# Kernel optimization log

Measured on AMD Instinct MI355X. Metric: run time of the kernel, lower is better.

Reference implementation:

```python
import jax, jax.numpy as jnp
import numpy as np

B, K, D, NH = 4096, 32, 1024, 16
HD = D // NH
LN_EPS = 1e-5
RMS_EPS = 1e-6


def layernorm(x, g, b):
    mu = jnp.mean(x, axis=-1, keepdims=True)
    var = jnp.mean((x - mu) ** 2, axis=-1, keepdims=True)
    return (x - mu) * jax.lax.rsqrt(var + LN_EPS) * g + b


def rmsnorm(x, g):
    ms = jnp.mean(x ** 2, axis=-1, keepdims=True)
    return x * jax.lax.rsqrt(ms + RMS_EPS) * g


def setup_inputs() -> dict:
    key = jax.random.key(0)
    ks = jax.random.split(key, 12)
    s = 0.02
    inp = {
        "query": jax.random.normal(ks[0], (B, D), jnp.float32),
        "point_features": jax.random.normal(ks[1], (B, K, D), jnp.float32),
        "lnq_g": jnp.ones((D,), jnp.float32),
        "lnq_b": jnp.zeros((D,), jnp.float32),
        "lnkv_g": jnp.ones((D,), jnp.float32),
        "lnkv_b": jnp.zeros((D,), jnp.float32),
        "Wq": jax.random.normal(ks[2], (D, D), jnp.float32) * s,
        "bq": jnp.zeros((D,), jnp.float32),
        "Wk": jax.random.normal(ks[3], (D, D), jnp.float32) * s,
        "bk": jnp.zeros((D,), jnp.float32),
        "Wv": jax.random.normal(ks[4], (D, D), jnp.float32) * s,
        "bv": jnp.zeros((D,), jnp.float32),
        "rmsq_g": jnp.ones((D,), jnp.float32),
        "rmsk_g": jnp.ones((D,), jnp.float32),
        "Wo": jax.random.normal(ks[5], (D, D), jnp.float32) * s,
        "bo": jnp.zeros((D,), jnp.float32),
        "mlpn_g": jnp.ones((D,), jnp.float32),
        "mlpn_b": jnp.zeros((D,), jnp.float32),
        "W1": jax.random.normal(ks[6], (D, 4 * D), jnp.float32) * s,
        "b1": jnp.zeros((4 * D,), jnp.float32),
        "W2": jax.random.normal(ks[7], (4 * D, D), jnp.float32) * s,
        "b2": jnp.zeros((D,), jnp.float32),
    }
    return inp


def reference(query, point_features, lnq_g, lnq_b, lnkv_g, lnkv_b,
              Wq, bq, Wk, bk, Wv, bv, rmsq_g, rmsk_g, Wo, bo,
              mlpn_g, mlpn_b, W1, b1, W2, b2):
    q_in = layernorm(query, lnq_g, lnq_b)            # [B, D]
    kv_in = layernorm(point_features, lnkv_g, lnkv_b)  # [B, K, D]

    q = rmsnorm(q_in @ Wq + bq, rmsq_g)              # [B, D]
    k = rmsnorm(kv_in @ Wk + bk, rmsk_g)             # [B, K, D]
    v = kv_in @ Wv + bv                               # [B, K, D]

    # Faithful to original: raw row-major reshape [B,K,D] -> [B,NH,K,HD]
    qh = q.reshape(B, NH, HD)                         # [B, NH, HD] (q_len = 1)
    kh = k.reshape(B, NH, K, HD)
    vh = v.reshape(B, NH, K, HD)

    scores = jnp.einsum('bhd,bhkd->bhk', qh, kh) / np.sqrt(HD).astype(np.float32)
    attn = jax.nn.softmax(scores, axis=-1)            # [B, NH, K]
    out = jnp.einsum('bhk,bhkd->bhd', attn, vh)       # [B, NH, HD]

    # Faithful: transpose(1,2) then reshape -> [B, HD, NH] -> [B, D]
    out = jnp.transpose(out, (0, 2, 1)).reshape(B, D)
    out = (out @ Wo + bo) + query                     # residual

    h = layernorm(out, mlpn_g, mlpn_b)
    mlp_out = (jax.nn.gelu(h @ W1 + b1, approximate=False) @ W2) + b2
    return out + mlp_out
```

## Files before the change

### kernel.cpp

```cpp
#include <hip/hip_runtime.h>
#include <stdint.h>

#define DEVI __device__ __forceinline__

typedef unsigned short u16;
typedef short s8v __attribute__((ext_vector_type(8)));
typedef float f4v __attribute__((ext_vector_type(4)));
typedef u16 u16x4 __attribute__((ext_vector_type(4)));

DEVI u16 f2bf(float f) {
  unsigned u = __float_as_uint(f);
  u += 0x7fffu + ((u >> 16) & 1u);
  return (u16)(u >> 16);
}
DEVI float bf2f(u16 h) { return __uint_as_float(((unsigned)h) << 16); }

DEVI void gload16(const void* g, void* l) {
  __builtin_amdgcn_global_load_lds(
      (const __attribute__((address_space(1))) void*)(uintptr_t)g,
      (__attribute__((address_space(3))) void*)(uintptr_t)l, 16, 0, 0);
}

__global__ __launch_bounds__(256) void transpose_w(const float* __restrict__ W,
                                                   u16* __restrict__ Wt, int R, int C) {
  __shared__ float tile[32][33];
  const int tx = threadIdx.x & 31, ty = threadIdx.x >> 5;
  const int r0 = blockIdx.y * 32, c0 = blockIdx.x * 32;
#pragma unroll
  for (int i = 0; i < 4; ++i)
    tile[ty + 8 * i][tx] = W[(size_t)(r0 + ty + 8 * i) * C + c0 + tx];
  __syncthreads();
#pragma unroll
  for (int i = 0; i < 4; ++i)
    Wt[(size_t)(c0 + ty + 8 * i) * R + r0 + tx] = f2bf(tile[tx][ty + 8 * i]);
}

__global__ __launch_bounds__(256) void ln_rows(const float* __restrict__ x,
                                               const float* __restrict__ g,
                                               const float* __restrict__ bsh,
                                               u16* __restrict__ y) {
  const size_t row = blockIdx.x;
  const int t = threadIdx.x;
  float4 v = ((const float4*)(x + row * 1024))[t];
  float s = v.x + v.y + v.z + v.w;
  float q = v.x * v.x + v.y * v.y + v.z * v.z + v.w * v.w;
#pragma unroll
  for (int m = 1; m < 64; m <<= 1) { s += __shfl_xor(s, m); q += __shfl_xor(q, m); }
  __shared__ float sh[8];
  if ((t & 63) == 0) { sh[t >> 6] = s; sh[4 + (t >> 6)] = q; }
  __syncthreads();
  s = sh[0] + sh[1] + sh[2] + sh[3];
  q = sh[4] + sh[5] + sh[6] + sh[7];
  const float mu = s * (1.f / 1024.f);
  const float var = q * (1.f / 1024.f) - mu * mu;
  const float rs = rsqrtf(var + 1e-5f);
  const int c = t * 4;
  const float in[4] = {v.x, v.y, v.z, v.w};
  u16x4 o;
#pragma unroll
  for (int i = 0; i < 4; ++i) o[i] = f2bf((in[i] - mu) * rs * g[c + i] + bsh[c + i]);
  *(u16x4*)(y + row * 1024 + c) = o;
}

__global__ __launch_bounds__(256) void qrms_k(const float* __restrict__ x,
                                              const float* __restrict__ gq,
                                              u16* __restrict__ y) {
  const size_t row = blockIdx.x;
  const int t = threadIdx.x;
  float4 v = ((const float4*)(x + row * 1024))[t];
  float q = v.x * v.x + v.y * v.y + v.z * v.z + v.w * v.w;
#pragma unroll
  for (int m = 1; m < 64; m <<= 1) q += __shfl_xor(q, m);
  __shared__ float sh[4];
  if ((t & 63) == 0) sh[t >> 6] = q;
  __syncthreads();
  q = sh[0] + sh[1] + sh[2] + sh[3];
  const float rs = rsqrtf(q * (1.f / 1024.f) + 1e-6f) * 0.125f;
  const int c = t * 4;
  const float in[4] = {v.x, v.y, v.z, v.w};
  u16x4 o;
#pragma unroll
  for (int i = 0; i < 4; ++i) o[i] = f2bf(in[i] * rs * gq[c + i]);
  *(u16x4*)(y + row * 1024 + c) = o;
}

template <int EPI>
__global__ __launch_bounds__(512, 2) void gemm256(
    const u16* __restrict__ A, const u16* __restrict__ Bt,
    const float* __restrict__ biasK, const float* __restrict__ biasV,
    const float* __restrict__ gcol, u16* __restrict__ CK, u16* __restrict__ CV,
    float* __restrict__ rowssq, int M, int N, int K, int RB) {
  __shared__ u16 lds[4][16384];
  const int t = threadIdx.x;
  const int lane = t & 63;
  const int wave = t >> 6;
  const int wm = wave >> 2, wn = wave & 3;
  const int fr = lane & 15, kq = lane >> 4;

  const int bid = blockIdx.x;
  const int cpx = gridDim.x >> 3;
  const int swz = (bid & 7) * cpx + (bid >> 3);
  const int rb = swz % RB, cb = swz / RB;
  const size_t row0 = (size_t)rb * 256, col0 = (size_t)cb * 256;

  f4v acc[8][4];
#pragma unroll
  for (int i = 0; i < 8; ++i)
#pragma unroll
    for (int n = 0; n < 4; ++n) acc[i][n] = (f4v){0.f, 0.f, 0.f, 0.f};

  const u16* Ag0 = A + (row0 + (t >> 2)) * (size_t)K + (t & 3) * 8;
  const u16* Ag1 = Ag0 + (size_t)128 * K;
  const u16* Bg0 = Bt + (col0 + (t >> 2)) * (size_t)K + (t & 3) * 8;
  const u16* Bg1 = Bg0 + (size_t)128 * K;

  const int NT = K >> 5;

#pragma unroll
  for (int tt = 0; tt < 3; ++tt) {
    u16* sA = &lds[tt][0];
    u16* sB = &lds[tt][8192];
    gload16(Ag0 + tt * 32, sA + t * 8);
    gload16(Ag1 + tt * 32, sA + 4096 + t * 8);
    gload16(Bg0 + tt * 32, sB + t * 8);
    gload16(Bg1 + tt * 32, sB + 4096 + t * 8);
  }

#pragma unroll 4
  for (int T = 0; T < NT; ++T) {
    asm volatile("s_waitcnt vmcnt(8)" ::: "memory");
    __builtin_amdgcn_s_barrier();
    __builtin_amdgcn_sched_barrier(0);
    const u16* sA = &lds[T & 3][0];
    const u16* sB = &lds[T & 3][8192];
    s8v a[4], b[4];
#pragma unroll
    for (int m = 0; m < 4; ++m)
      a[m] = *(const s8v*)&sA[(wm * 128 + m * 16 + fr) * 32 + kq * 8];
#pragma unroll
    for (int n = 0; n < 4; ++n)
      b[n] = *(const s8v*)&sB[(wn * 64 + n * 16 + fr) * 32 + kq * 8];
    if (T + 3 < NT) {
      u16* dA = &lds[(T + 3) & 3][0];
      gload16(Ag0 + (T + 3) * 32, dA + t * 8);
      gload16(Ag1 + (T + 3) * 32, dA + 4096 + t * 8);
    }
    __builtin_amdgcn_s_setprio(1);
#pragma unroll
    for (int m = 0; m < 4; ++m)
#pragma unroll
      for (int n = 0; n < 4; ++n)
        acc[m][n] = __builtin_amdgcn_mfma_f32_16x16x32_bf16(a[m], b[n], acc[m][n], 0, 0, 0);
    __builtin_amdgcn_s_setprio(0);
    __builtin_amdgcn_s_barrier();
#pragma unroll
    for (int m = 0; m < 4; ++m)
      a[m] = *(const s8v*)&sA[(wm * 128 + 64 + m * 16 + fr) * 32 + kq * 8];
    if (T + 3 < NT) {
      u16* dB = &lds[(T + 3) & 3][8192];
      gload16(Bg0 + (T + 3) * 32, dB + t * 8);
      gload16(Bg1 + (T + 3) * 32, dB + 4096 + t * 8);
    }
    __builtin_amdgcn_s_setprio(1);
#pragma unroll
    for (int m = 0; m < 4; ++m)
#pragma unroll
      for (int n = 0; n < 4; ++n)
        acc[4 + m][n] = __builtin_amdgcn_mfma_f32_16x16x32_bf16(a[m], b[n], acc[4 + m][n], 0, 0, 0);
    __builtin_amdgcn_s_setprio(0);
  }

  const int kq4 = kq * 4;
  if (EPI == 0) {
    const bool isK = (col0 < 1024);
    if (isK) {
#pragma unroll
      for (int ai = 0; ai < 8; ++ai) {
        int cols[4];
        float bb[4], gg[4];
#pragma unroll
        for (int n = 0; n < 4; ++n) {
          cols[n] = (int)col0 + wn * 64 + n * 16 + fr;
          bb[n] = biasK[cols[n]];
          gg[n] = gcol[cols[n]];
        }
#pragma unroll
        for (int r = 0; r < 4; ++r) {
          const size_t grow = row0 + wm * 128 + ai * 16 + kq4 + r;
          float v[4];
#pragma unroll
          for (int n = 0; n < 4; ++n) v[n] = acc[ai][n][r] + bb[n];
          float s = v[0] * v[0] + v[1] * v[1] + v[2] * v[2] + v[3] * v[3];
          s += __shfl_xor(s, 1);
          s += __shfl_xor(s, 2);
          s += __shfl_xor(s, 4);
          s += __shfl_xor(s, 8);
          if (fr == 0) atomicAdd(&rowssq[grow], s);
#pragma unroll
          for (int n = 0; n < 4; ++n)
            CK[grow * 1024 + cols[n]] = f2bf(v[n] * gg[n]);
        }
      }
    } else {
#pragma unroll
      for (int ai = 0; ai < 8; ++ai) {
        int cols[4];
        float bb[4];
#pragma unroll
        for (int n = 0; n < 4; ++n) {
          cols[n] = (int)col0 - 1024 + wn * 64 + n * 16 + fr;
          bb[n] = biasV[cols[n]];
        }
#pragma unroll
        for (int r = 0; r < 4; ++r) {
          const size_t grow = row0 + wm * 128 + ai * 16 + kq4 + r;
#pragma unroll
          for (int n = 0; n < 4; ++n)
            CV[grow * 1024 + cols[n]] = f2bf(acc[ai][n][r] + bb[n]);
        }
      }
    }
  } else {
#pragma unroll
    for (int ai = 0; ai < 8; ++ai) {
      int cols[4];
      float bb[4];
#pragma unroll
      for (int n = 0; n < 4; ++n) {
        cols[n] = (int)col0 + wn * 64 + n * 16 + fr;
        bb[n] = biasK[cols[n]];
      }
#pragma unroll
      for (int r = 0; r < 4; ++r) {
        const size_t grow = row0 + wm * 128 + ai * 16 + kq4 + r;
#pragma unroll
        for (int n = 0; n < 4; ++n) {
          const float x = acc[ai][n][r] + bb[n];
          CK[grow * (size_t)N + cols[n]] = f2bf(0.5f * x * (1.f + erff(x * 0.70710678118654752f)));
        }
      }
    }
  }
}

template <int EPI>
__global__ __launch_bounds__(256) void gemm_bt(
    const u16* __restrict__ A, const u16* __restrict__ Bt,
    const float* __restrict__ bias, const float* __restrict__ gcol,
    void* __restrict__ Cv, const float* __restrict__ extra,
    float* __restrict__ rowssq, int M, int N, int K) {
  __shared__ u16 As[128 * 32];
  __shared__ u16 Bs[128 * 32];
  const int t = threadIdx.x;
  const int lane = t & 63;
  const int wave = t >> 6;
  const int wr = wave >> 1, wc = wave & 1;
  const size_t row0 = (size_t)blockIdx.y * 128;
  const size_t col0 = (size_t)blockIdx.x * 128;

  f4v acc[4][4];
#pragma unroll
  for (int m = 0; m < 4; ++m)
#pragma unroll
    for (int n = 0; n < 4; ++n) acc[m][n] = (f4v){0.f, 0.f, 0.f, 0.f};

  const int sr = t >> 2;
  const int sc = (t & 3) * 8;
  const u16* Ag = A + (row0 + sr) * (size_t)K + sc;
  const u16* Bg = Bt + (col0 + sr) * (size_t)K + sc;
  u16* Al = &As[sr * 32 + sc];
  u16* Bl = &Bs[sr * 32 + sc];
  const int fr = lane & 15;
  const int kg = (lane >> 4) * 8;

  for (int k0 = 0; k0 < K; k0 += 32) {
    gload16(Ag + k0, Al);
    gload16(Ag + k0 + (size_t)64 * K, Al + 64 * 32);
    gload16(Bg + k0, Bl);
    gload16(Bg + k0 + (size_t)64 * K, Bl + 64 * 32);
    __syncthreads();
    s8v a[4], b[4];
#pragma unroll
    for (int m = 0; m < 4; ++m)
      a[m] = *(const s8v*)&As[(wr * 64 + m * 16 + fr) * 32 + kg];
#pragma unroll
    for (int n = 0; n < 4; ++n)
      b[n] = *(const s8v*)&Bs[(wc * 64 + n * 16 + fr) * 32 + kg];
#pragma unroll
    for (int m = 0; m < 4; ++m)
#pragma unroll
      for (int n = 0; n < 4; ++n)
        acc[m][n] = __builtin_amdgcn_mfma_f32_16x16x32_bf16(a[m], b[n], acc[m][n], 0, 0, 0);
    __syncthreads();
  }

  const int rg = (lane >> 4) * 4;
#pragma unroll
  for (int m = 0; m < 4; ++m) {
    int cols[4];
    float bvals[4];
#pragma unroll
    for (int n = 0; n < 4; ++n) {
      cols[n] = (int)col0 + wc * 64 + n * 16 + fr;
      bvals[n] = bias[cols[n]];
    }
#pragma unroll
    for (int r = 0; r < 4; ++r) {
      const size_t grow = row0 + wr * 64 + m * 16 + rg + r;
      float v[4];
#pragma unroll
      for (int n = 0; n < 4; ++n) v[n] = acc[m][n][r] + bvals[n];
#pragma unroll
      for (int n = 0; n < 4; ++n) {
        const size_t idx = grow * (size_t)N + cols[n];
        if (EPI == 0) {
          ((float*)Cv)[idx] = v[n];
        } else if (EPI == 3) {
          ((float*)Cv)[idx] = v[n] + extra[idx];
        } else if (EPI == 4) {
          const float x = v[n];
          ((u16*)Cv)[idx] = f2bf(0.5f * x * (1.f + erff(x * 0.70710678118654752f)));
        }
      }
    }
  }
}

__global__ __launch_bounds__(256) void attn_k(const u16* __restrict__ qf,
                                              const u16* __restrict__ kmat,
                                              const float* __restrict__ kssq,
                                              const u16* __restrict__ vmat,
                                              u16* __restrict__ ao) {
  const int lb = blockIdx.x;
  const int t = threadIdx.x;
  const int wave = t >> 6, lane = t & 63;
  const int j = lane & 31, half = lane >> 5;
  __shared__ float po[64][17];
#pragma unroll
  for (int hi = 0; hi < 4; ++hi) {
    const int h = wave * 4 + hi;
    const int krow = lb * 32 + 2 * h + (j >> 4);
    const u16* kp = kmat + (size_t)krow * 1024 + (j & 15) * 64 + half * 32;
    const u16* qp = qf + (size_t)lb * 1024 + h * 64 + half * 32;
    float s = 0.f;
#pragma unroll
    for (int cc = 0; cc < 4; ++cc) {
      s8v qv = *(const s8v*)(qp + cc * 8);
      s8v kv = *(const s8v*)(kp + cc * 8);
#pragma unroll
      for (int e = 0; e < 8; ++e) s += bf2f((u16)qv[e]) * bf2f((u16)kv[e]);
    }
    s += __shfl_xor(s, 32);
    s *= rsqrtf(kssq[krow] * (1.f / 1024.f) + 1e-6f);
    float mx = s;
#pragma unroll
    for (int m = 16; m >= 1; m >>= 1) mx = fmaxf(mx, __shfl_xor(mx, m));
    const float pe = __expf(s - mx);
    float sum = pe;
#pragma unroll
    for (int m = 16; m >= 1; m >>= 1) sum += __shfl_xor(sum, m);
    const float pr = pe / sum;
    float o = 0.f;
#pragma unroll
    for (int jj = 0; jj < 32; ++jj) {
      const int vrow = lb * 32 + 2 * h + (jj >> 4);
      const float vv = bf2f(vmat[(size_t)vrow * 1024 + (jj & 15) * 64 + lane]);
      o += __shfl(pr, jj) * vv;
    }
    po[lane][h] = o;
  }
  __syncthreads();
  const int c = t * 4;
  u16x4 o4;
#pragma unroll
  for (int i = 0; i < 4; ++i) o4[i] = f2bf(po[(c + i) >> 4][(c + i) & 15]);
  *(u16x4*)(ao + (size_t)lb * 1024 + c) = o4;
}

extern "C" void kernel_launch(void* const* d_in, const int* in_sizes, int n_in,
                              void* d_out, int out_size, void* d_ws, size_t ws_size,
                              hipStream_t stream) {
  const float* query  = (const float*)d_in[0];
  const float* pf     = (const float*)d_in[1];
  const float* lnq_g  = (const float*)d_in[2];
  const float* lnq_b  = (const float*)d_in[3];
  const float* lnkv_g = (const float*)d_in[4];
  const float* lnkv_b = (const float*)d_in[5];
  const float* Wq     = (const float*)d_in[6];
  const float* bq     = (const float*)d_in[7];
  const float* Wk     = (const float*)d_in[8];
  const float* bk     = (const float*)d_in[9];
  const float* Wv     = (const float*)d_in[10];
  const float* bv     = (const float*)d_in[11];
  const float* rmsq_g = (const float*)d_in[12];
  const float* rmsk_g = (const float*)d_in[13];
  const float* Wo     = (const float*)d_in[14];
  const float* bo     = (const float*)d_in[15];
  const float* mlpn_g = (const float*)d_in[16];
  const float* mlpn_b = (const float*)d_in[17];
  const float* W1     = (const float*)d_in[18];
  const float* b1     = (const float*)d_in[19];
  const float* W2     = (const float*)d_in[20];
  const float* b2     = (const float*)d_in[21];
  float* out = (float*)d_out;

  char* p = (char*)d_ws;
  auto alloc = [&](size_t n) {
    char* r = p;
    p += (n + 255) & ~(size_t)255;
    return r;
  };

  u16* Wqt = (u16*)alloc((size_t)1024 * 1024 * 2);
  u16* KVt = (u16*)alloc((size_t)2048 * 1024 * 2);
  u16* Wot = (u16*)alloc((size_t)1024 * 1024 * 2);
  u16* W1t = (u16*)alloc((size_t)1024 * 4096 * 2);
  u16* W2t = (u16*)alloc((size_t)4096 * 1024 * 2);
  u16* qln = (u16*)alloc((size_t)4096 * 1024 * 2);
  float* qtmp = (float*)alloc((size_t)4096 * 1024 * 4);
  u16* qfin = (u16*)alloc((size_t)4096 * 1024 * 2);
  u16* attn_o = (u16*)alloc((size_t)4096 * 1024 * 2);
  float* outbuf = (float*)alloc((size_t)4096 * 1024 * 4);
  u16* hbuf = (u16*)alloc((size_t)4096 * 1024 * 2);
  u16* mid = (u16*)alloc((size_t)4096 * 4096 * 2);

  const size_t used = (size_t)(p - (char*)d_ws);
  int NC = 4;
  while (NC < 64) {
    size_t rows_try = (size_t)131072 / NC;
    if (used + 3 * (rows_try * 2048 + 256) + rows_try * 4 + 256 <= ws_size) break;
    NC *= 2;
  }
  const size_t rows = (size_t)131072 / NC;
  u16* kvln = (u16*)alloc(rows * 2048);
  u16* kmat = (u16*)alloc(rows * 2048);
  u16* vmat = (u16*)alloc(rows * 2048);
  float* kssq = (float*)alloc(rows * 4);

  transpose_w<<<dim3(32, 32), 256, 0, stream>>>(Wq, Wqt, 1024, 1024);
  transpose_w<<<dim3(32, 32), 256, 0, stream>>>(Wk, KVt, 1024, 1024);
  transpose_w<<<dim3(32, 32), 256, 0, stream>>>(Wv, KVt + (size_t)1024 * 1024, 1024, 1024);
  transpose_w<<<dim3(32, 32), 256, 0, stream>>>(Wo, Wot, 1024, 1024);
  transpose_w<<<dim3(128, 32), 256, 0, stream>>>(W1, W1t, 1024, 4096);
  transpose_w<<<dim3(32, 128), 256, 0, stream>>>(W2, W2t, 4096, 1024);

  ln_rows<<<4096, 256, 0, stream>>>(query, lnq_g, lnq_b, qln);
  gemm_bt<0><<<dim3(8, 32), 256, 0, stream>>>(qln, Wqt, bq, nullptr, qtmp, nullptr,
                                              nullptr, 4096, 1024, 1024);
  qrms_k<<<4096, 256, 0, stream>>>(qtmp, rmsq_g, qfin);

  const int bpc = 4096 / NC;
  for (int c = 0; c < NC; ++c) {
    ln_rows<<<(unsigned)rows, 256, 0, stream>>>(pf + (size_t)c * rows * 1024, lnkv_g,
                                                lnkv_b, kvln);
    hipMemsetAsync(kssq, 0, rows * 4, stream);
    const int RB = (int)(rows / 256);
    gemm256<0><<<RB * 8, 512, 0, stream>>>(kvln, KVt, bk, bv, rmsk_g, kmat, vmat,
                                           kssq, (int)rows, 2048, 1024, RB);
    attn_k<<<bpc, 256, 0, stream>>>(qfin + (size_t)c * bpc * 1024, kmat, kssq, vmat,
                                    attn_o + (size_t)c * bpc * 1024);
  }

  gemm_bt<3><<<dim3(8, 32), 256, 0, stream>>>(attn_o, Wot, bo, nullptr, outbuf, query,
                                              nullptr, 4096, 1024, 1024);
  ln_rows<<<4096, 256, 0, stream>>>(outbuf, mlpn_g, mlpn_b, hbuf);
  gemm256<1><<<16 * 16, 512, 0, stream>>>(hbuf, W1t, b1, nullptr, nullptr, mid, nullptr,
                                          nullptr, 4096, 4096, 1024, 16);
  gemm_bt<3><<<dim3(8, 32), 256, 0, stream>>>(mid, W2t, b2, nullptr, out, outbuf,
                                              nullptr, 4096, 1024, 4096);
}
```

Measured before the change: 1.190 ms.

## Fuse q RMS norm into attention, drop KV chunking, split-K the W2 GEMM

Folds the q RMSnorm into the Q projection epilogue, which writes bf16 plus per-row sum of squares via atomics, and into the attention kernel, which applies the gain and rsqrt. This removes the fp32 qtmp round trip and the qrms kernel. The point-feature path now runs as one full-size pass instead of a loop of chunks. The zeroing of the sum-of-squares buffer moves into the layernorm kernel, and the gemm256 tile order becomes row-major with branch-free clamped prefetch. The W2 GEMM is split-K into two partial outputs that a new combine kernel sums with bias and residual. All of this trades extra workspace (full-size KV buffers, two fp32 partials) and float atomics for fewer launches and more parallelism.

```diff
diff --git a/kernel.cpp b/kernel.cpp
--- a/kernel.cpp
+++ b/kernel.cpp
@@ -38,9 +38,11 @@
 __global__ __launch_bounds__(256) void ln_rows(const float* __restrict__ x,
                                                const float* __restrict__ g,
                                                const float* __restrict__ bsh,
-                                               u16* __restrict__ y) {
+                                               u16* __restrict__ y,
+                                               float* __restrict__ zbuf) {
   const size_t row = blockIdx.x;
   const int t = threadIdx.x;
+  if (zbuf && t == 0) zbuf[row] = 0.f;
   float4 v = ((const float4*)(x + row * 1024))[t];
   float s = v.x + v.y + v.z + v.w;
   float q = v.x * v.x + v.y * v.y + v.z * v.z + v.w * v.w;
@@ -62,34 +64,12 @@
   *(u16x4*)(y + row * 1024 + c) = o;
 }
 
-__global__ __launch_bounds__(256) void qrms_k(const float* __restrict__ x,
-                                              const float* __restrict__ gq,
-                                              u16* __restrict__ y) {
-  const size_t row = blockIdx.x;
-  const int t = threadIdx.x;
-  float4 v = ((const float4*)(x + row * 1024))[t];
-  float q = v.x * v.x + v.y * v.y + v.z * v.z + v.w * v.w;
-#pragma unroll
-  for (int m = 1; m < 64; m <<= 1) q += __shfl_xor(q, m);
-  __shared__ float sh[4];
-  if ((t & 63) == 0) sh[t >> 6] = q;
-  __syncthreads();
-  q = sh[0] + sh[1] + sh[2] + sh[3];
-  const float rs = rsqrtf(q * (1.f / 1024.f) + 1e-6f) * 0.125f;
-  const int c = t * 4;
-  const float in[4] = {v.x, v.y, v.z, v.w};
-  u16x4 o;
-#pragma unroll
-  for (int i = 0; i < 4; ++i) o[i] = f2bf(in[i] * rs * gq[c + i]);
-  *(u16x4*)(y + row * 1024 + c) = o;
-}
-
 template <int EPI>
 __global__ __launch_bounds__(512, 2) void gemm256(
     const u16* __restrict__ A, const u16* __restrict__ Bt,
     const float* __restrict__ biasK, const float* __restrict__ biasV,
     const float* __restrict__ gcol, u16* __restrict__ CK, u16* __restrict__ CV,
-    float* __restrict__ rowssq, int M, int N, int K, int RB) {
+    float* __restrict__ rowssq, int M, int N, int K, int RB, int CB) {
   __shared__ u16 lds[4][16384];
   const int t = threadIdx.x;
   const int lane = t & 63;
@@ -100,7 +80,7 @@
   const int bid = blockIdx.x;
   const int cpx = gridDim.x >> 3;
   const int swz = (bid & 7) * cpx + (bid >> 3);
-  const int rb = swz % RB, cb = swz / RB;
+  const int rb = swz / CB, cb = swz % CB;
   const size_t row0 = (size_t)rb * 256, col0 = (size_t)cb * 256;
 
   f4v acc[8][4];
@@ -133,6 +113,7 @@
     __builtin_amdgcn_sched_barrier(0);
     const u16* sA = &lds[T & 3][0];
     const u16* sB = &lds[T & 3][8192];
+    const int Ts = (T + 3 < NT) ? T + 3 : NT - 1;
     s8v a[4], b[4];
 #pragma unroll
     for (int m = 0; m < 4; ++m)
@@ -140,10 +121,10 @@
 #pragma unroll
     for (int n = 0; n < 4; ++n)
       b[n] = *(const s8v*)&sB[(wn * 64 + n * 16 + fr) * 32 + kq * 8];
-    if (T + 3 < NT) {
+    {
       u16* dA = &lds[(T + 3) & 3][0];
-      gload16(Ag0 + (T + 3) * 32, dA + t * 8);
-      gload16(Ag1 + (T + 3) * 32, dA + 4096 + t * 8);
+      gload16(Ag0 + Ts * 32, dA + t * 8);
+      gload16(Ag1 + Ts * 32, dA + 4096 + t * 8);
     }
     __builtin_amdgcn_s_setprio(1);
 #pragma unroll
@@ -156,10 +137,10 @@
 #pragma unroll
     for (int m = 0; m < 4; ++m)
       a[m] = *(const s8v*)&sA[(wm * 128 + 64 + m * 16 + fr) * 32 + kq * 8];
-    if (T + 3 < NT) {
+    {
       u16* dB = &lds[(T + 3) & 3][8192];
-      gload16(Bg0 + (T + 3) * 32, dB + t * 8);
-      gload16(Bg1 + (T + 3) * 32, dB + 4096 + t * 8);
+      gload16(Bg0 + Ts * 32, dB + t * 8);
+      gload16(Bg1 + Ts * 32, dB + 4096 + t * 8);
     }
     __builtin_amdgcn_s_setprio(1);
 #pragma unroll
@@ -257,6 +238,8 @@
   const int wr = wave >> 1, wc = wave & 1;
   const size_t row0 = (size_t)blockIdx.y * 128;
   const size_t col0 = (size_t)blockIdx.x * 128;
+  int Ksub = K, koff = 0;
+  if (EPI == 6) { Ksub = K / gridDim.z; koff = blockIdx.z * Ksub; }
 
   f4v acc[4][4];
 #pragma unroll
@@ -266,14 +249,14 @@
 
   const int sr = t >> 2;
   const int sc = (t & 3) * 8;
-  const u16* Ag = A + (row0 + sr) * (size_t)K + sc;
-  const u16* Bg = Bt + (col0 + sr) * (size_t)K + sc;
+  const u16* Ag = A + (row0 + sr) * (size_t)K + koff + sc;
+  const u16* Bg = Bt + (col0 + sr) * (size_t)K + koff + sc;
   u16* Al = &As[sr * 32 + sc];
   u16* Bl = &Bs[sr * 32 + sc];
   const int fr = lane & 15;
   const int kg = (lane >> 4) * 8;
 
-  for (int k0 = 0; k0 < K; k0 += 32) {
+  for (int k0 = 0; k0 < Ksub; k0 += 32) {
     gload16(Ag + k0, Al);
     gload16(Ag + k0 + (size_t)64 * K, Al + 64 * 32);
     gload16(Bg + k0, Bl);
@@ -294,6 +277,8 @@
     __syncthreads();
   }
 
+  float* Cp = (float*)Cv;
+  if (EPI == 6) Cp += (size_t)blockIdx.z * M * (size_t)N;
   const int rg = (lane >> 4) * 4;
 #pragma unroll
   for (int m = 0; m < 4; ++m) {
@@ -302,7 +287,7 @@
 #pragma unroll
     for (int n = 0; n < 4; ++n) {
       cols[n] = (int)col0 + wc * 64 + n * 16 + fr;
-      bvals[n] = bias[cols[n]];
+      bvals[n] = (EPI == 6) ? 0.f : bias[cols[n]];
     }
 #pragma unroll
     for (int r = 0; r < 4; ++r) {
@@ -310,16 +295,23 @@
       float v[4];
 #pragma unroll
       for (int n = 0; n < 4; ++n) v[n] = acc[m][n][r] + bvals[n];
+      if (EPI == 5) {
+        float s = v[0] * v[0] + v[1] * v[1] + v[2] * v[2] + v[3] * v[3];
+        s += __shfl_xor(s, 1);
+        s += __shfl_xor(s, 2);
+        s += __shfl_xor(s, 4);
+        s += __shfl_xor(s, 8);
+        if (fr == 0) atomicAdd(&rowssq[grow], s);
+      }
 #pragma unroll
       for (int n = 0; n < 4; ++n) {
         const size_t idx = grow * (size_t)N + cols[n];
-        if (EPI == 0) {
-          ((float*)Cv)[idx] = v[n];
-        } else if (EPI == 3) {
-          ((float*)Cv)[idx] = v[n] + extra[idx];
-        } else if (EPI == 4) {
-          const float x = v[n];
-          ((u16*)Cv)[idx] = f2bf(0.5f * x * (1.f + erff(x * 0.70710678118654752f)));
+        if (EPI == 3) {
+          Cp[idx] = v[n] + extra[idx];
+        } else if (EPI == 5) {
+          ((u16*)Cv)[idx] = f2bf(v[n]);
+        } else if (EPI == 6) {
+          Cp[idx] = v[n];
         }
       }
     }
@@ -330,11 +322,14 @@
                                               const u16* __restrict__ kmat,
                                               const float* __restrict__ kssq,
                                               const u16* __restrict__ vmat,
+                                              const float* __restrict__ gq,
+                                              const float* __restrict__ qssq,
                                               u16* __restrict__ ao) {
   const int lb = blockIdx.x;
   const int t = threadIdx.x;
   const int wave = t >> 6, lane = t & 63;
   const int j = lane & 31, half = lane >> 5;
+  const float rq = rsqrtf(qssq[lb] * (1.f / 1024.f) + 1e-6f) * 0.125f;
   __shared__ float po[64][17];
 #pragma unroll
   for (int hi = 0; hi < 4; ++hi) {
@@ -342,16 +337,18 @@
     const int krow = lb * 32 + 2 * h + (j >> 4);
     const u16* kp = kmat + (size_t)krow * 1024 + (j & 15) * 64 + half * 32;
     const u16* qp = qf + (size_t)lb * 1024 + h * 64 + half * 32;
+    const float* gqp = gq + h * 64 + half * 32;
     float s = 0.f;
 #pragma unroll
     for (int cc = 0; cc < 4; ++cc) {
       s8v qv = *(const s8v*)(qp + cc * 8);
       s8v kv = *(const s8v*)(kp + cc * 8);
 #pragma unroll
-      for (int e = 0; e < 8; ++e) s += bf2f((u16)qv[e]) * bf2f((u16)kv[e]);
+      for (int e = 0; e < 8; ++e)
+        s += bf2f((u16)qv[e]) * gqp[cc * 8 + e] * bf2f((u16)kv[e]);
     }
     s += __shfl_xor(s, 32);
-    s *= rsqrtf(kssq[krow] * (1.f / 1024.f) + 1e-6f);
+    s *= rsqrtf(kssq[krow] * (1.f / 1024.f) + 1e-6f) * rq;
     float mx = s;
 #pragma unroll
     for (int m = 16; m >= 1; m >>= 1) mx = fmaxf(mx, __shfl_xor(mx, m));
@@ -375,6 +372,24 @@
 #pragma unroll
   for (int i = 0; i < 4; ++i) o4[i] = f2bf(po[(c + i) >> 4][(c + i) & 15]);
   *(u16x4*)(ao + (size_t)lb * 1024 + c) = o4;
+}
+
+__global__ __launch_bounds__(256) void combine_k(const float* __restrict__ p0,
+                                                 const float* __restrict__ p1,
+                                                 const float* __restrict__ b2,
+                                                 const float* __restrict__ resid,
+                                                 float* __restrict__ out) {
+  const int i = blockIdx.x * 256 + threadIdx.x;
+  float4 a = ((const float4*)p0)[i];
+  float4 b = ((const float4*)p1)[i];
+  float4 r = ((const float4*)resid)[i];
+  float4 bb = ((const float4*)b2)[i & 255];
+  float4 o;
+  o.x = a.x + b.x + r.x + bb.x;
+  o.y = a.y + b.y + r.y + bb.y;
+  o.z = a.z + b.z + r.z + bb.z;
+  o.w = a.w + b.w + r.w + bb.w;
+  ((float4*)out)[i] = o;
 }
 
 extern "C" void kernel_launch(void* const* d_in, const int* in_sizes, int n_in,
@@ -417,25 +432,18 @@
   u16* W1t = (u16*)alloc((size_t)1024 * 4096 * 2);
   u16* W2t = (u16*)alloc((size_t)4096 * 1024 * 2);
   u16* qln = (u16*)alloc((size_t)4096 * 1024 * 2);
-  float* qtmp = (float*)alloc((size_t)4096 * 1024 * 4);
-  u16* qfin = (u16*)alloc((size_t)4096 * 1024 * 2);
+  u16* qpre = (u16*)alloc((size_t)4096 * 1024 * 2);
+  float* qssq = (float*)alloc((size_t)4096 * 4);
   u16* attn_o = (u16*)alloc((size_t)4096 * 1024 * 2);
   float* outbuf = (float*)alloc((size_t)4096 * 1024 * 4);
   u16* hbuf = (u16*)alloc((size_t)4096 * 1024 * 2);
   u16* mid = (u16*)alloc((size_t)4096 * 4096 * 2);
-
-  const size_t used = (size_t)(p - (char*)d_ws);
-  int NC = 4;
-  while (NC < 64) {
-    size_t rows_try = (size_t)131072 / NC;
-    if (used + 3 * (rows_try * 2048 + 256) + rows_try * 4 + 256 <= ws_size) break;
-    NC *= 2;
-  }
-  const size_t rows = (size_t)131072 / NC;
-  u16* kvln = (u16*)alloc(rows * 2048);
-  u16* kmat = (u16*)alloc(rows * 2048);
-  u16* vmat = (u16*)alloc(rows * 2048);
-  float* kssq = (float*)alloc(rows * 4);
+  float* w2p = (float*)alloc((size_t)2 * 4096 * 1024 * 4);
+  const size_t ROWS = 131072;
+  u16* kvln = (u16*)alloc(ROWS * 2048);
+  u16* kmat = (u16*)alloc(ROWS * 2048);
+  u16* vmat = (u16*)alloc(ROWS * 2048);
+  float* kssq = (float*)alloc(ROWS * 4);
 
   transpose_w<<<dim3(32, 32), 256, 0, stream>>>(Wq, Wqt, 1024, 1024);
   transpose_w<<<dim3(32, 32), 256, 0, stream>>>(Wk, KVt, 1024, 1024);
@@ -444,28 +452,21 @@
   transpose_w<<<dim3(128, 32), 256, 0, stream>>>(W1, W1t, 1024, 4096);
   transpose_w<<<dim3(32, 128), 256, 0, stream>>>(W2, W2t, 4096, 1024);
 
-  ln_rows<<<4096, 256, 0, stream>>>(query, lnq_g, lnq_b, qln);
-  gemm_bt<0><<<dim3(8, 32), 256, 0, stream>>>(qln, Wqt, bq, nullptr, qtmp, nullptr,
-                                              nullptr, 4096, 1024, 1024);
-  qrms_k<<<4096, 256, 0, stream>>>(qtmp, rmsq_g, qfin);
-
-  const int bpc = 4096 / NC;
-  for (int c = 0; c < NC; ++c) {
-    ln_rows<<<(unsigned)rows, 256, 0, stream>>>(pf + (size_t)c * rows * 1024, lnkv_g,
-                                                lnkv_b, kvln);
-    hipMemsetAsync(kssq, 0, rows * 4, stream);
-    const int RB = (int)(rows / 256);
-    gemm256<0><<<RB * 8, 512, 0, stream>>>(kvln, KVt, bk, bv, rmsk_g, kmat, vmat,
-                                           kssq, (int)rows, 2048, 1024, RB);
-    attn_k<<<bpc, 256, 0, stream>>>(qfin + (size_t)c * bpc * 1024, kmat, kssq, vmat,
-                                    attn_o + (size_t)c * bpc * 1024);
-  }
+  ln_rows<<<4096, 256, 0, stream>>>(query, lnq_g, lnq_b, qln, qssq);
+  gemm_bt<5><<<dim3(8, 32), 256, 0, stream>>>(qln, Wqt, bq, nullptr, qpre, nullptr,
+                                              qssq, 4096, 1024, 1024);
+
+  ln_rows<<<(unsigned)ROWS, 256, 0, stream>>>(pf, lnkv_g, lnkv_b, kvln, kssq);
+  gemm256<0><<<512 * 8, 512, 0, stream>>>(kvln, KVt, bk, bv, rmsk_g, kmat, vmat,
+                                          kssq, (int)ROWS, 2048, 1024, 512, 8);
+  attn_k<<<4096, 256, 0, stream>>>(qpre, kmat, kssq, vmat, rmsq_g, qssq, attn_o);
 
   gemm_bt<3><<<dim3(8, 32), 256, 0, stream>>>(attn_o, Wot, bo, nullptr, outbuf, query,
                                               nullptr, 4096, 1024, 1024);
-  ln_rows<<<4096, 256, 0, stream>>>(outbuf, mlpn_g, mlpn_b, hbuf);
+  ln_rows<<<4096, 256, 0, stream>>>(outbuf, mlpn_g, mlpn_b, hbuf, nullptr);
   gemm256<1><<<16 * 16, 512, 0, stream>>>(hbuf, W1t, b1, nullptr, nullptr, mid, nullptr,
-                                          nullptr, 4096, 4096, 1024, 16);
-  gemm_bt<3><<<dim3(8, 32), 256, 0, stream>>>(mid, W2t, b2, nullptr, out, outbuf,
-                                              nullptr, 4096, 1024, 4096);
-}
+                                          nullptr, 4096, 4096, 1024, 16, 16);
+  gemm_bt<6><<<dim3(8, 32, 2), 256, 0, stream>>>(mid, W2t, nullptr, nullptr, w2p,
+                                                 nullptr, nullptr, 4096, 1024, 4096);
+  combine_k<<<4096, 256, 0, stream>>>(w2p, w2p + (size_t)4096 * 1024, b2, outbuf, out);
+}
```

Result: faster. 1.091 ms (-8.3%).
